# Optimization experiments

Hardware: AMD Instinct MI355X
Metric: run time of the kernel (lower is better)

Reference implementation:

```python
import jax, jax.numpy as jnp
import numpy as np

NAF, NBF, DT = 64, 32, 1
B, GROUP = 2000, 100
P = B * GROUP

def _lin(key, din, dout):
    kw, kb = jax.random.split(key)
    return (jax.random.normal(kw, (din, dout), jnp.float32) * 0.02,
            jax.random.normal(kb, (dout,), jnp.float32) * 0.01)

def setup_inputs() -> dict:
    key = jax.random.key(0)
    ks = jax.random.split(key, 12)
    pairs = jax.random.normal(ks[0], (P, 2 * NAF + NBF), jnp.float32)
    idx_pairs = jnp.full((B,), GROUP, dtype=jnp.int32)
    ref_feats = jax.random.normal(ks[1], (B, 32), jnp.float32)
    aw, ab = _lin(ks[2], NAF, 128)
    bw, bb = _lin(ks[3], NBF, 128)
    p1w, p1b = _lin(ks[4], 384, 512)
    p2w, p2b = _lin(ks[5], 512, 256)
    p3w, p3b = _lin(ks[6], 256, 1024)
    f1w, f1b = _lin(ks[7], 1024, 512)
    f2w, f2b = _lin(ks[8], 512, 32)
    f3w, f3b = _lin(ks[9], 32, DT)
    return dict(pairs=pairs, idx_pairs=idx_pairs, ref_feats=ref_feats,
                aw=aw, ab=ab, bw=bw, bb=bb,
                p1w=p1w, p1b=p1b, p2w=p2w, p2b=p2b, p3w=p3w, p3b=p3b,
                f1w=f1w, f1b=f1b, f2w=f2w, f2b=f2b, f3w=f3w, f3b=f3b)

def reference(pairs, idx_pairs, ref_feats,
              aw, ab, bw, bb,
              p1w, p1b, p2w, p2b, p3w, p3b,
              f1w, f1b, f2w, f2b, f3w, f3b):
    relu = jax.nn.relu
    a1 = relu(pairs[:, :NAF] @ aw + ab)            # [P,128]
    a2 = relu(pairs[:, NAF:2 * NAF] @ aw + ab)     # [P,128]
    be = relu(pairs[:, 2 * NAF:] @ bw + bb)        # [P,128]
    h = jnp.concatenate([a1, a2, be], axis=1)      # [P,384]
    h = relu(h @ p1w + p1b)
    h = relu(h @ p2w + p2b)
    x = h @ p3w + p3b                              # [P,1024]
    nb = idx_pairs.shape[0]
    seg = jnp.repeat(jnp.arange(nb, dtype=jnp.int32), idx_pairs,
                     total_repeat_length=x.shape[0])
    sums = jax.ops.segment_sum(x, seg, num_segments=nb)
    h_pair = sums / idx_pairs[:, None].astype(x.dtype)  # segment mean [B,1024]
    h = relu(h_pair @ f1w + f1b)
    h = relu(h @ f2w + f2b)
    return h @ f3w + f3b                           # [B,1]
```

## Files before the change

kernel.cpp:

```cpp
#include <hip/hip_runtime.h>
#include <cstdint>
#include <cstddef>


typedef __bf16 bf16;
typedef __attribute__((ext_vector_type(8))) __bf16 bf16x8;
typedef __attribute__((ext_vector_type(4))) __bf16 bf16x4;
typedef __attribute__((ext_vector_type(4))) float floatx4;

#define GRP 100
#define NWIN 3125

#define WOFF_AW 0
#define WOFF_BW 8192
#define WOFF_P1 12288
#define WOFF_P2 208896
#define WOFF_P3 339968
#define WOFF_F1 602112
#define WOFF_F2 1126400
#define WOFF_HS 1142784

#define LSTR_P  168
#define LSTR_H  392
#define LSTR_H2 136
#define LSTR_MS 264

static __device__ __forceinline__ floatx4 mfma16(bf16x8 a, bf16x8 b, floatx4 c) {
  return __builtin_amdgcn_mfma_f32_16x16x32_bf16(a, b, c, 0, 0, 0);
}

__global__ __launch_bounds__(256) void pack_lds(
    const float* __restrict__ aw, const float* __restrict__ bw,
    const float* __restrict__ p1w, const float* __restrict__ p2w,
    const float* __restrict__ p3w, const float* __restrict__ f1w,
    const float* __restrict__ f2w, bf16* __restrict__ wpk) {
  __shared__ float t[32][65];
  const int tid = threadIdx.x;
  int b = blockIdx.x;

  if (b < 550) {
    const float* src; int dstoff, K, N, tt;
    if (b < 4)        { src = aw;  dstoff = WOFF_AW; K = 64;   N = 128;  tt = b; }
    else if (b < 6)   { src = bw;  dstoff = WOFF_BW; K = 32;   N = 128;  tt = b - 4; }
    else if (b < 102) { src = p1w; dstoff = WOFF_P1; K = 384;  N = 512;  tt = b - 6; }
    else if (b < 166) { src = p2w; dstoff = WOFF_P2; K = 512;  N = 256;  tt = b - 102; }
    else if (b < 294) { src = p3w; dstoff = WOFF_P3; K = 256;  N = 1024; tt = b - 166; }
    else              { src = f1w; dstoff = WOFF_F1; K = 1024; N = 512;  tt = b - 294; }
    const int KT = K >> 5;
    const int kt = tt % KT;
    const int n0 = (tt / KT) * 64;
    for (int i = tid; i < 2048; i += 256) {
      int r = i >> 6, c = i & 63;
      t[r][c] = src[(size_t)(kt * 32 + r) * N + n0 + c];
    }
    __syncthreads();
    const int nc = n0 >> 7, nl0 = n0 & 127;
    bf16* dst = wpk + dstoff + ((size_t)(nc * KT + kt) * 128 + nl0) * 32;
    int o = tid * 8;
    int nl = o >> 5, kk = o & 31;
    bf16x8 v;
#pragma unroll
    for (int i = 0; i < 8; ++i) v[i] = (bf16)t[kk + i][nl];
    *(bf16x8*)(dst + nl * 32 + kk) = v;
  } else {
    const int kt = b - 550;
    for (int i = tid; i < 1024; i += 256) {
      int r = i >> 5, c = i & 31;
      t[r][c] = f2w[(size_t)(kt * 32 + r) * 32 + c];
    }
    __syncthreads();
    if (tid < 128) {
      int o = tid * 8;
      int nl = o >> 5, kk = o & 31;
      bf16x8 v;
#pragma unroll
      for (int i = 0; i < 8; ++i) v[i] = (bf16)t[kk + i][nl];
      *(bf16x8*)(wpk + WOFF_F2 + kt * 1024 + nl * 32 + kk) = v;
    }
  }
}

static __device__ __forceinline__ void kstep2(const bf16* __restrict__ Ab,
                                              int astride, int acol,
                                              const bf16* __restrict__ b0p,
                                              const bf16* __restrict__ b1p,
                                              floatx4* acc, int lm, int lq) {
  bf16x8 b0 = *(const bf16x8*)b0p;
  bf16x8 b1 = *(const bf16x8*)b1p;
#pragma unroll
  for (int mt = 0; mt < 4; ++mt) {
    bf16x8 a = *(const bf16x8*)(Ab + (mt * 16 + lm) * astride + acol + lq * 8);
    acc[mt * 2]     = mfma16(a, b0, acc[mt * 2]);
    acc[mt * 2 + 1] = mfma16(a, b1, acc[mt * 2 + 1]);
  }
}

static __device__ __forceinline__ void epi2(const floatx4* acc,
                                            const float* __restrict__ bias,
                                            bf16* dst, int dstride, int w,
                                            int lm, int lq) {
#pragma unroll
  for (int mt = 0; mt < 4; ++mt)
#pragma unroll
    for (int j = 0; j < 2; ++j) {
      int col = (w + 4 * j) * 16 + lm;
      float bv = bias[col];
      floatx4 c = acc[mt * 2 + j];
#pragma unroll
      for (int r = 0; r < 4; ++r) {
        float v = c[r] + bv;
        v = v > 0.f ? v : 0.f;
        dst[(mt * 16 + lq * 4 + r) * dstride + col] = (bf16)v;
      }
    }
}

__global__ __launch_bounds__(256, 2) void seg_kernel(
    const float* __restrict__ pairs, const float* __restrict__ ab,
    const float* __restrict__ bb, const float* __restrict__ p1b,
    const float* __restrict__ p2b, const bf16* __restrict__ wpk,
    float* __restrict__ hsum) {
  __shared__ __align__(16) bf16 hbuf[64 * LSTR_H];
  __shared__ __align__(16) bf16 pbuf[64 * LSTR_P];

  const int tid = threadIdx.x;
  const int w = tid >> 6;
  const int lane = tid & 63;
  const int lm = lane & 15;
  const int lq = lane >> 4;
  const int blk = blockIdx.x;

  {
    const float4* src = (const float4*)(pairs + (size_t)blk * (64 * 160));
    for (int i = tid; i < 64 * 40; i += 256) {
      int row = i / 40;
      int c4 = (i - row * 40) * 4;
      float4 v = src[i];
      bf16x4 o = {(bf16)v.x, (bf16)v.y, (bf16)v.z, (bf16)v.w};
      *(bf16x4*)(pbuf + row * LSTR_P + c4) = o;
    }
  }
  __syncthreads();

  const floatx4 fz = {0.f, 0.f, 0.f, 0.f};
  floatx4 acc[8];
  floatx4 acc3[16];

#pragma unroll
  for (int t = 0; t < 8; ++t) acc[t] = fz;
#pragma unroll
  for (int kt = 0; kt < 2; ++kt)
    kstep2(pbuf, LSTR_P, kt * 32,
           wpk + WOFF_AW + ((size_t)(kt * 128 + w * 16 + lm)) * 32 + lq * 8,
           wpk + WOFF_AW + ((size_t)(kt * 128 + (w + 4) * 16 + lm)) * 32 + lq * 8,
           acc, lm, lq);
  epi2(acc, ab, hbuf, LSTR_H, w, lm, lq);
#pragma unroll
  for (int t = 0; t < 8; ++t) acc[t] = fz;
#pragma unroll
  for (int kt = 0; kt < 2; ++kt)
    kstep2(pbuf, LSTR_P, 64 + kt * 32,
           wpk + WOFF_AW + ((size_t)(kt * 128 + w * 16 + lm)) * 32 + lq * 8,
           wpk + WOFF_AW + ((size_t)(kt * 128 + (w + 4) * 16 + lm)) * 32 + lq * 8,
           acc, lm, lq);
  epi2(acc, ab, hbuf + 128, LSTR_H, w, lm, lq);
#pragma unroll
  for (int t = 0; t < 8; ++t) acc[t] = fz;
  kstep2(pbuf, LSTR_P, 128,
         wpk + WOFF_BW + ((size_t)(w * 16 + lm)) * 32 + lq * 8,
         wpk + WOFF_BW + ((size_t)((w + 4) * 16 + lm)) * 32 + lq * 8,
         acc, lm, lq);
  epi2(acc, bb, hbuf + 256, LSTR_H, w, lm, lq);

  __syncthreads();

#pragma unroll
  for (int t = 0; t < 16; ++t) acc3[t] = fz;

  for (int nc = 0; nc < 4; ++nc) {
#pragma unroll
    for (int t = 0; t < 8; ++t) acc[t] = fz;

    {
      const bf16* bp = wpk + WOFF_P1 +
          ((size_t)(nc * 12) * 128 + w * 16 + lm) * 32 + lq * 8;
      bf16x8 bs0[2], bs1[2];
      bf16x8 an[2][4];
#pragma unroll
      for (int q = 0; q < 2; ++q) {
        bs0[q] = *(const bf16x8*)(bp + (size_t)q * 4096);
        bs1[q] = *(const bf16x8*)(bp + (size_t)q * 4096 + 2048);
#pragma unroll
        for (int mt = 0; mt < 4; ++mt)
          an[q][mt] = *(const bf16x8*)(hbuf + (mt * 16 + lm) * LSTR_H +
                                       q * 32 + lq * 8);
      }
#pragma unroll
      for (int kt = 0; kt < 12; ++kt) {
        bf16x8 b0 = bs0[kt & 1], b1 = bs1[kt & 1];
        bf16x8 ac[4];
#pragma unroll
        for (int mt = 0; mt < 4; ++mt) ac[mt] = an[kt & 1][mt];
        if (kt < 10) {
          bs0[kt & 1] = *(const bf16x8*)(bp + (size_t)(kt + 2) * 4096);
          bs1[kt & 1] = *(const bf16x8*)(bp + (size_t)(kt + 2) * 4096 + 2048);
#pragma unroll
          for (int mt = 0; mt < 4; ++mt)
            an[kt & 1][mt] = *(const bf16x8*)(hbuf + (mt * 16 + lm) * LSTR_H +
                                              (kt + 2) * 32 + lq * 8);
        }
        asm volatile("" ::: "memory");
        __builtin_amdgcn_s_setprio(1);
#pragma unroll
        for (int mt = 0; mt < 4; ++mt) {
          acc[mt * 2]     = mfma16(ac[mt], b0, acc[mt * 2]);
          acc[mt * 2 + 1] = mfma16(ac[mt], b1, acc[mt * 2 + 1]);
        }
        __builtin_amdgcn_s_setprio(0);
      }
    }
    __syncthreads();
    epi2(acc, p1b + nc * 128, pbuf, LSTR_H2, w, lm, lq);
    __syncthreads();

    {
      const bf16* bp = wpk + WOFF_P2 +
          ((size_t)(((w >> 1) * 16 + nc * 4) * 128 + (w & 1) * 64 + lm)) * 32 +
          lq * 8;
      bf16x8 bs[2][4];
      bf16x8 an[2][4];
#pragma unroll
      for (int q = 0; q < 2; ++q) {
#pragma unroll
        for (int j = 0; j < 4; ++j)
          bs[q][j] = *(const bf16x8*)(bp + (size_t)q * 4096 + j * 512);
#pragma unroll
        for (int mt = 0; mt < 4; ++mt)
          an[q][mt] = *(const bf16x8*)(pbuf + (mt * 16 + lm) * LSTR_H2 +
                                       q * 32 + lq * 8);
      }
#pragma unroll
      for (int kt2 = 0; kt2 < 4; ++kt2) {
        bf16x8 bc[4], ac[4];
#pragma unroll
        for (int j = 0; j < 4; ++j) bc[j] = bs[kt2 & 1][j];
#pragma unroll
        for (int mt = 0; mt < 4; ++mt) ac[mt] = an[kt2 & 1][mt];
        if (kt2 < 2) {
#pragma unroll
          for (int j = 0; j < 4; ++j)
            bs[kt2 & 1][j] =
                *(const bf16x8*)(bp + (size_t)(kt2 + 2) * 4096 + j * 512);
#pragma unroll
          for (int mt = 0; mt < 4; ++mt)
            an[kt2 & 1][mt] = *(const bf16x8*)(pbuf + (mt * 16 + lm) * LSTR_H2 +
                                               (kt2 + 2) * 32 + lq * 8);
        }
        asm volatile("" ::: "memory");
        __builtin_amdgcn_s_setprio(1);
#pragma unroll
        for (int mt = 0; mt < 4; ++mt)
#pragma unroll
          for (int j = 0; j < 4; ++j)
            acc3[mt * 4 + j] = mfma16(ac[mt], bc[j], acc3[mt * 4 + j]);
        __builtin_amdgcn_s_setprio(0);
      }
    }
  }

  const int s0 = (64 * blk) / 100;
  const int sp = (s0 + 1) * 100 - 64 * blk;
  floatx4 msk[4];
#pragma unroll
  for (int mt = 0; mt < 4; ++mt)
#pragma unroll
    for (int r = 0; r < 4; ++r)
      msk[mt][r] = (mt * 16 + lq * 4 + r < sp) ? 1.f : 0.f;

#pragma unroll
  for (int s = 0; s < 4; ++s) {
    int cl = w * 64 + s * 16 + lm;
    float bv = p2b[cl];
    float tot = 0.f, cs0 = 0.f;
#pragma unroll
    for (int mt = 0; mt < 4; ++mt) {
      floatx4 c = acc3[mt * 4 + s];
#pragma unroll
      for (int r = 0; r < 4; ++r) {
        float v = c[r] + bv;
        v = v > 0.f ? v : 0.f;
        tot += v;
        cs0 = fmaf(v, msk[mt][r], cs0);
      }
    }
    float cs1 = tot - cs0;
    cs0 += __shfl_xor(cs0, 16, 64);
    cs0 += __shfl_xor(cs0, 32, 64);
    cs1 += __shfl_xor(cs1, 16, 64);
    cs1 += __shfl_xor(cs1, 32, 64);
    if (lq == 0) {
      hsum[(size_t)(2 * blk) * 256 + cl]     = cs0;
      hsum[(size_t)(2 * blk + 1) * 256 + cl] = cs1;
    }
  }
}

__global__ __launch_bounds__(512, 2) void tail_kernel(
    const bf16* __restrict__ wpk, const float* __restrict__ hsum,
    const int* __restrict__ idxp, const float* __restrict__ p3b,
    const float* __restrict__ f1b, const float* __restrict__ f2b,
    const float* __restrict__ f3w, const float* __restrict__ f3b,
    float* __restrict__ out) {
  __shared__ __align__(16) bf16 ms[16 * LSTR_MS];
  __shared__ __align__(16) bf16 hp[16 * 1032];
  __shared__ __align__(16) bf16 h2s[16 * 520];
  __shared__ __align__(16) bf16 h3s[16 * 40];

  const int tid = threadIdx.x;
  const int w = tid >> 6;
  const int lane = tid & 63;
  const int lm = lane & 15;
  const int lq = lane >> 4;
  const int r0 = blockIdx.x * 16;
  const floatx4 fz = {0.f, 0.f, 0.f, 0.f};

  for (int i = tid; i < 16 * 64; i += 512) {
    int row = i >> 6, c4 = i & 63;
    int seg = r0 + row;
    int b_lo = (100 * seg) >> 6;
    int b_hi = (100 * seg + 99) >> 6;
    float4 sa = {0.f, 0.f, 0.f, 0.f};
    for (int b = b_lo; b <= b_hi; ++b) {
      int slot = (64 * b >= 100 * seg) ? 0 : 1;
      float4 v = *(const float4*)(hsum + (size_t)(2 * b + slot) * 256 + c4 * 4);
      sa.x += v.x; sa.y += v.y; sa.z += v.z; sa.w += v.w;
    }
    float inv = 1.f / (float)idxp[seg];
    bf16x4 o = {(bf16)(sa.x * inv), (bf16)(sa.y * inv),
                (bf16)(sa.z * inv), (bf16)(sa.w * inv)};
    *(bf16x4*)(ms + row * LSTR_MS + c4 * 4) = o;
  }
  __syncthreads();

#pragma unroll
  for (int nt2 = 0; nt2 < 4; ++nt2) {
    floatx4 a2[2];
    a2[0] = fz; a2[1] = fz;
#pragma unroll
    for (int kt = 0; kt < 8; ++kt) {
      bf16x8 a = *(const bf16x8*)(ms + lm * LSTR_MS + kt * 32 + lq * 8);
#pragma unroll
      for (int j = 0; j < 2; ++j) {
        bf16x8 b = *(const bf16x8*)(wpk + WOFF_P3 +
            ((size_t)((w * 8 + kt) * 128 + (nt2 * 2 + j) * 16 + lm)) * 32 +
            lq * 8);
        a2[j] = mfma16(a, b, a2[j]);
      }
    }
#pragma unroll
    for (int j = 0; j < 2; ++j) {
      int col = w * 128 + (nt2 * 2 + j) * 16 + lm;
      float bv = p3b[col];
#pragma unroll
      for (int r = 0; r < 4; ++r)
        hp[(lq * 4 + r) * 1032 + col] = (bf16)(a2[j][r] + bv);
    }
  }
  __syncthreads();

  {
    floatx4 a4[4];
#pragma unroll
    for (int j = 0; j < 4; ++j) a4[j] = fz;
#pragma unroll 8
    for (int kt = 0; kt < 32; ++kt) {
      bf16x8 a = *(const bf16x8*)(hp + lm * 1032 + kt * 32 + lq * 8);
#pragma unroll
      for (int j = 0; j < 4; ++j) {
        bf16x8 b = *(const bf16x8*)(wpk + WOFF_F1 +
            ((size_t)(((w >> 1) * 32 + kt) * 128 + (w & 1) * 64 + j * 16 + lm)) * 32 +
            lq * 8);
        a4[j] = mfma16(a, b, a4[j]);
      }
    }
#pragma unroll
    for (int j = 0; j < 4; ++j) {
      int col = w * 64 + j * 16 + lm;
      float bv = f1b[col];
#pragma unroll
      for (int r = 0; r < 4; ++r) {
        float v = a4[j][r] + bv;
        v = v > 0.f ? v : 0.f;
        h2s[(lq * 4 + r) * 520 + col] = (bf16)v;
      }
    }
  }
  __syncthreads();

  if (w < 2) {
    floatx4 c2 = fz;
#pragma unroll
    for (int kt = 0; kt < 16; ++kt) {
      bf16x8 a = *(const bf16x8*)(h2s + lm * 520 + kt * 32 + lq * 8);
      bf16x8 b = *(const bf16x8*)(wpk + WOFF_F2 +
                    ((size_t)(kt * 32 + w * 16 + lm)) * 32 + lq * 8);
      c2 = mfma16(a, b, c2);
    }
    int col = w * 16 + lm;
    float bv = f2b[col];
#pragma unroll
    for (int r = 0; r < 4; ++r) {
      float v = c2[r] + bv;
      v = v > 0.f ? v : 0.f;
      h3s[(lq * 4 + r) * 40 + col] = (bf16)v;
    }
  }
  __syncthreads();
  if (w == 0) {
    float ps = 0.f;
#pragma unroll
    for (int jj = 0; jj < 8; ++jj)
      ps += (float)h3s[lm * 40 + lq * 8 + jj] * f3w[lq * 8 + jj];
    ps += __shfl_xor(ps, 16, 64);
    ps += __shfl_xor(ps, 32, 64);
    if (lq == 0) out[r0 + lm] = ps + f3b[0];
  }
}

extern "C" void kernel_launch(void* const* d_in, const int* in_sizes, int n_in,
                              void* d_out, int out_size, void* d_ws,
                              size_t ws_size, hipStream_t stream) {
  (void)in_sizes; (void)n_in; (void)out_size; (void)ws_size;
  const float* pairs = (const float*)d_in[0];
  const int*   idxp  = (const int*)d_in[1];
  const float* aw  = (const float*)d_in[3];
  const float* ab  = (const float*)d_in[4];
  const float* bw  = (const float*)d_in[5];
  const float* bb  = (const float*)d_in[6];
  const float* p1w = (const float*)d_in[7];
  const float* p1b = (const float*)d_in[8];
  const float* p2w = (const float*)d_in[9];
  const float* p2b = (const float*)d_in[10];
  const float* p3w = (const float*)d_in[11];
  const float* p3b = (const float*)d_in[12];
  const float* f1w = (const float*)d_in[13];
  const float* f1b = (const float*)d_in[14];
  const float* f2w = (const float*)d_in[15];
  const float* f2b = (const float*)d_in[16];
  const float* f3w = (const float*)d_in[17];
  const float* f3b = (const float*)d_in[18];

  bf16* wpk = (bf16*)d_ws;
  float* hsum = (float*)(wpk + WOFF_HS);

  pack_lds<<<566, 256, 0, stream>>>(aw, bw, p1w, p2w, p3w, f1w, f2w, wpk);
  seg_kernel<<<NWIN, 256, 0, stream>>>(pairs, ab, bb, p1b, p2b, wpk, hsum);
  tail_kernel<<<125, 512, 0, stream>>>(wpk, hsum, idxp, p3b, f1b, f2b, f3w,
                                       f3b, (float*)d_out);
}
```

Measured before the change: 410.1 us.

## Software-pipeline weight loads with inline asm and explicit vmcnt waits

```diff
diff --git a/kernel.cpp b/kernel.cpp
--- a/kernel.cpp
+++ b/kernel.cpp
@@ -28,6 +28,25 @@
 static __device__ __forceinline__ floatx4 mfma16(bf16x8 a, bf16x8 b, floatx4 c) {
   return __builtin_amdgcn_mfma_f32_16x16x32_bf16(a, b, c, 0, 0, 0);
 }
+
+static __device__ __forceinline__ void gload(floatx4& d, const bf16* p) {
+  asm volatile("global_load_dwordx4 %0, %1, off" : "=v"(d) : "v"(p));
+}
+static __device__ __forceinline__ bf16x8 bc8(floatx4 v) {
+  return __builtin_bit_cast(bf16x8, v);
+}
+
+#define VMW(N)                                         \
+  do {                                                 \
+    asm volatile("s_waitcnt vmcnt(" #N ")");           \
+    __builtin_amdgcn_sched_barrier(0);                 \
+  } while (0)
+
+#define SYNCL()                                        \
+  do {                                                 \
+    asm volatile("s_waitcnt lgkmcnt(0)" ::: "memory"); \
+    __builtin_amdgcn_s_barrier();                      \
+  } while (0)
 
 __global__ __launch_bounds__(256) void pack_lds(
     const float* __restrict__ aw, const float* __restrict__ bw,
@@ -115,6 +134,25 @@
     }
 }
 
+static __device__ __forceinline__ void epi2v(const floatx4* acc, float bv0,
+                                             float bv1, bf16* dst, int dstride,
+                                             int w, int lm, int lq) {
+#pragma unroll
+  for (int mt = 0; mt < 4; ++mt)
+#pragma unroll
+    for (int j = 0; j < 2; ++j) {
+      int col = (w + 4 * j) * 16 + lm;
+      float bv = j ? bv1 : bv0;
+      floatx4 c = acc[mt * 2 + j];
+#pragma unroll
+      for (int r = 0; r < 4; ++r) {
+        float v = c[r] + bv;
+        v = v > 0.f ? v : 0.f;
+        dst[(mt * 16 + lq * 4 + r) * dstride + col] = (bf16)v;
+      }
+    }
+}
+
 __global__ __launch_bounds__(256, 2) void seg_kernel(
     const float* __restrict__ pairs, const float* __restrict__ ab,
     const float* __restrict__ bb, const float* __restrict__ p1b,
@@ -140,7 +178,7 @@
       *(bf16x4*)(pbuf + row * LSTR_P + c4) = o;
     }
   }
-  __syncthreads();
+  SYNCL();
 
   const floatx4 fz = {0.f, 0.f, 0.f, 0.f};
   floatx4 acc[8];
@@ -172,45 +210,72 @@
          acc, lm, lq);
   epi2(acc, bb, hbuf + 256, LSTR_H, w, lm, lq);
 
-  __syncthreads();
+  float p1bv0[4], p1bv1[4], p2bv[4];
+#pragma unroll
+  for (int nc = 0; nc < 4; ++nc) {
+    p1bv0[nc] = p1b[nc * 128 + w * 16 + lm];
+    p1bv1[nc] = p1b[nc * 128 + (w + 4) * 16 + lm];
+  }
+#pragma unroll
+  for (int s = 0; s < 4; ++s) p2bv[s] = p2b[w * 64 + s * 16 + lm];
+  asm volatile("" : "+v"(p1bv0[0]), "+v"(p1bv0[1]), "+v"(p1bv0[2]),
+                    "+v"(p1bv0[3]), "+v"(p1bv1[0]), "+v"(p1bv1[1]),
+                    "+v"(p1bv1[2]), "+v"(p1bv1[3]), "+v"(p2bv[0]),
+                    "+v"(p2bv[1]), "+v"(p2bv[2]), "+v"(p2bv[3]));
+
+  const bf16* bp0 = wpk + WOFF_P1 + ((size_t)(w * 16 + lm)) * 32 + lq * 8;
+  const bf16* bp2 = wpk + WOFF_P2 +
+      ((size_t)(((w >> 1) * 16) * 128 + (w & 1) * 64 + lm)) * 32 + lq * 8;
+
+  floatx4 p1r0[4], p1r1[4];
+  floatx4 p2r[3][4];
+
+#pragma unroll
+  for (int q = 0; q < 3; ++q) {
+    gload(p1r0[q], bp0 + (size_t)q * 4096);
+    gload(p1r1[q], bp0 + (size_t)q * 4096 + 2048);
+  }
+  SYNCL();
 
 #pragma unroll
   for (int t = 0; t < 16; ++t) acc3[t] = fz;
 
+#pragma unroll
   for (int nc = 0; nc < 4; ++nc) {
 #pragma unroll
     for (int t = 0; t < 8; ++t) acc[t] = fz;
 
     {
-      const bf16* bp = wpk + WOFF_P1 +
-          ((size_t)(nc * 12) * 128 + w * 16 + lm) * 32 + lq * 8;
-      bf16x8 bs0[2], bs1[2];
       bf16x8 an[2][4];
 #pragma unroll
-      for (int q = 0; q < 2; ++q) {
-        bs0[q] = *(const bf16x8*)(bp + (size_t)q * 4096);
-        bs1[q] = *(const bf16x8*)(bp + (size_t)q * 4096 + 2048);
+      for (int q = 0; q < 2; ++q)
 #pragma unroll
         for (int mt = 0; mt < 4; ++mt)
           an[q][mt] = *(const bf16x8*)(hbuf + (mt * 16 + lm) * LSTR_H +
                                        q * 32 + lq * 8);
-      }
 #pragma unroll
       for (int kt = 0; kt < 12; ++kt) {
-        bf16x8 b0 = bs0[kt & 1], b1 = bs1[kt & 1];
         bf16x8 ac[4];
 #pragma unroll
         for (int mt = 0; mt < 4; ++mt) ac[mt] = an[kt & 1][mt];
         if (kt < 10) {
-          bs0[kt & 1] = *(const bf16x8*)(bp + (size_t)(kt + 2) * 4096);
-          bs1[kt & 1] = *(const bf16x8*)(bp + (size_t)(kt + 2) * 4096 + 2048);
 #pragma unroll
           for (int mt = 0; mt < 4; ++mt)
             an[kt & 1][mt] = *(const bf16x8*)(hbuf + (mt * 16 + lm) * LSTR_H +
                                               (kt + 2) * 32 + lq * 8);
         }
-        asm volatile("" ::: "memory");
+        if (kt < 9) {
+          gload(p1r0[(kt + 3) & 3], bp0 + (size_t)(nc * 12 + kt + 3) * 4096);
+          gload(p1r1[(kt + 3) & 3],
+                bp0 + (size_t)(nc * 12 + kt + 3) * 4096 + 2048);
+        }
+        if (kt < 9)       { VMW(6); }
+        else if (kt == 9) { VMW(4); }
+        else if (kt == 10){ VMW(2); }
+        else              { VMW(0); }
         __builtin_amdgcn_s_setprio(1);
+        bf16x8 b0 = bc8(p1r0[kt & 3]);
+        bf16x8 b1 = bc8(p1r1[kt & 3]);
 #pragma unroll
         for (int mt = 0; mt < 4; ++mt) {
           acc[mt * 2]     = mfma16(ac[mt], b0, acc[mt * 2]);
@@ -219,50 +284,59 @@
         __builtin_amdgcn_s_setprio(0);
       }
     }
-    __syncthreads();
-    epi2(acc, p1b + nc * 128, pbuf, LSTR_H2, w, lm, lq);
-    __syncthreads();
+
+#pragma unroll
+    for (int q = 0; q < 2; ++q)
+#pragma unroll
+      for (int j = 0; j < 4; ++j)
+        gload(p2r[q][j], bp2 + (size_t)(nc * 4 + q) * 4096 + j * 512);
+
+    SYNCL();
+    epi2v(acc, p1bv0[nc], p1bv1[nc], pbuf, LSTR_H2, w, lm, lq);
+    SYNCL();
 
     {
-      const bf16* bp = wpk + WOFF_P2 +
-          ((size_t)(((w >> 1) * 16 + nc * 4) * 128 + (w & 1) * 64 + lm)) * 32 +
-          lq * 8;
-      bf16x8 bs[2][4];
-      bf16x8 an[2][4];
-#pragma unroll
-      for (int q = 0; q < 2; ++q) {
-#pragma unroll
-        for (int j = 0; j < 4; ++j)
-          bs[q][j] = *(const bf16x8*)(bp + (size_t)q * 4096 + j * 512);
+      bf16x8 an2[2][4];
+#pragma unroll
+      for (int q = 0; q < 2; ++q)
 #pragma unroll
         for (int mt = 0; mt < 4; ++mt)
-          an[q][mt] = *(const bf16x8*)(pbuf + (mt * 16 + lm) * LSTR_H2 +
-                                       q * 32 + lq * 8);
-      }
+          an2[q][mt] = *(const bf16x8*)(pbuf + (mt * 16 + lm) * LSTR_H2 +
+                                        q * 32 + lq * 8);
 #pragma unroll
       for (int kt2 = 0; kt2 < 4; ++kt2) {
-        bf16x8 bc[4], ac[4];
-#pragma unroll
-        for (int j = 0; j < 4; ++j) bc[j] = bs[kt2 & 1][j];
-#pragma unroll
-        for (int mt = 0; mt < 4; ++mt) ac[mt] = an[kt2 & 1][mt];
+        bf16x8 ac[4];
+#pragma unroll
+        for (int mt = 0; mt < 4; ++mt) ac[mt] = an2[kt2 & 1][mt];
         if (kt2 < 2) {
 #pragma unroll
+          for (int mt = 0; mt < 4; ++mt)
+            an2[kt2 & 1][mt] = *(const bf16x8*)(pbuf + (mt * 16 + lm) * LSTR_H2 +
+                                                (kt2 + 2) * 32 + lq * 8);
+#pragma unroll
           for (int j = 0; j < 4; ++j)
-            bs[kt2 & 1][j] =
-                *(const bf16x8*)(bp + (size_t)(kt2 + 2) * 4096 + j * 512);
-#pragma unroll
-          for (int mt = 0; mt < 4; ++mt)
-            an[kt2 & 1][mt] = *(const bf16x8*)(pbuf + (mt * 16 + lm) * LSTR_H2 +
-                                               (kt2 + 2) * 32 + lq * 8);
+            gload(p2r[(kt2 + 2) % 3][j],
+                  bp2 + (size_t)(nc * 4 + kt2 + 2) * 4096 + j * 512);
         }
-        asm volatile("" ::: "memory");
+        if (kt2 == 1) {
+          const int ncn = (nc + 1) & 3;
+#pragma unroll
+          for (int q = 0; q < 3; ++q) {
+            gload(p1r0[q], bp0 + (size_t)(ncn * 12 + q) * 4096);
+            gload(p1r1[q], bp0 + (size_t)(ncn * 12 + q) * 4096 + 2048);
+          }
+        }
+        if (kt2 == 0)      { VMW(8); }
+        else if (kt2 == 1) { VMW(14); }
+        else if (kt2 == 2) { VMW(10); }
+        else               { VMW(6); }
         __builtin_amdgcn_s_setprio(1);
 #pragma unroll
         for (int mt = 0; mt < 4; ++mt)
 #pragma unroll
           for (int j = 0; j < 4; ++j)
-            acc3[mt * 4 + j] = mfma16(ac[mt], bc[j], acc3[mt * 4 + j]);
+            acc3[mt * 4 + j] =
+                mfma16(ac[mt], bc8(p2r[kt2 % 3][j]), acc3[mt * 4 + j]);
         __builtin_amdgcn_s_setprio(0);
       }
     }
@@ -280,7 +354,7 @@
 #pragma unroll
   for (int s = 0; s < 4; ++s) {
     int cl = w * 64 + s * 16 + lm;
-    float bv = p2b[cl];
+    float bv = p2bv[s];
     float tot = 0.f, cs0 = 0.f;
 #pragma unroll
     for (int mt = 0; mt < 4; ++mt) {
```

New measurement: 399.5 us. -2.6%, faster.
